# Performance work log

Measured on AMD Instinct MI355X. Metric: run time of the kernel, lower is better.

Reference implementation:

```python
import jax, jax.numpy as jnp
from jax import lax
import numpy as np

N, C, T, V = 32, 64, 300, 25   # batch, channels, frames, joints
INTER = 16                     # out_channels // coff_embedding (64//4)
NS = 3                         # num_subset
K = 9                          # temporal kernel size
EPS = 1e-5                     # torch BatchNorm2d default eps


def _bn(x, g, b):
    # training-mode BatchNorm2d over (N, T, V) per channel, biased variance
    m = x.mean(axis=(0, 2, 3), keepdims=True)
    v = x.var(axis=(0, 2, 3), keepdims=True)
    return (x - m) * lax.rsqrt(v + EPS) * g[None, :, None, None] + b[None, :, None, None]


def setup_inputs() -> dict:
    key = jax.random.key(0)
    ks = jax.random.split(key, 8)
    rn = lambda k, shape, sc=0.05: jax.random.normal(k, shape, jnp.float32) * sc
    x = jax.random.normal(ks[0], (N, C, T, V), jnp.float32)
    A = jax.random.uniform(ks[1], (NS, V, V), dtype=jnp.float32)
    PA = jnp.full((NS, V, V), 1e-6, jnp.float32)   # learned adjacency offset (init 1e-6)
    Wa = rn(ks[2], (NS, INTER, C)); ba = jnp.zeros((NS, INTER), jnp.float32)
    Wb = rn(ks[3], (NS, INTER, C)); bb = jnp.zeros((NS, INTER), jnp.float32)
    Wd = rn(ks[4], (NS, C, C));     bd = jnp.zeros((NS, C), jnp.float32)
    g1 = jnp.ones((C,), jnp.float32); b1 = jnp.zeros((C,), jnp.float32)
    Wt = rn(ks[5], (C, C, K, 1));   bt = jnp.zeros((C,), jnp.float32)
    g2 = jnp.ones((C,), jnp.float32); b2 = jnp.zeros((C,), jnp.float32)
    return dict(x=x, A=A, PA=PA, Wa=Wa, ba=ba, Wb=Wb, bb=bb, Wd=Wd, bd=bd,
                g1=g1, b1=b1, Wt=Wt, bt=bt, g2=g2, b2=b2)


def reference(x, A, PA, Wa, ba, Wb, bb, Wd, bd, g1, b1, Wt, bt, g2, b2):
    n, c, t, v = x.shape
    Au = A + PA                      # effective adjacency per subset, [NS,V,V]
    scale = 1.0 / (INTER * t)        # A1.size(-1)
    x_flat = x.reshape(n, c * t, v)  # [N, C*T, V]
    y = None
    for i in range(NS):
        # 1x1 convs -> embeddings, [N, INTER, T, V]
        a = jnp.einsum('nctv,oc->notv', x, Wa[i]) + ba[i][None, :, None, None]
        b = jnp.einsum('nctv,oc->notv', x, Wb[i]) + bb[i][None, :, None, None]
        A1 = a.transpose(0, 3, 1, 2).reshape(n, v, INTER * t)  # [N, V, INTER*T]
        A2 = b.reshape(n, INTER * t, v)                        # [N, INTER*T, V]
        attn = jax.nn.softmax(jnp.matmul(A1, A2) * scale, axis=-2) + Au[i]  # [N,V,V]
        z = jnp.matmul(x_flat, attn).reshape(n, c, t, v)       # aggregate over joints
        z = jnp.einsum('nctv,oc->notv', z, Wd[i]) + bd[i][None, :, None, None]
        y = z if y is None else y + z
    y = jax.nn.relu(_bn(y, g1, b1) + x)      # gcn bn + identity down + relu
    # temporal conv (9,1), pad (4,0), stride 1, then BN
    yc = lax.conv_general_dilated(y, Wt, window_strides=(1, 1),
                                  padding=((K // 2, K // 2), (0, 0)),
                                  dimension_numbers=('NCHW', 'OIHW', 'NCHW'))
    yc = _bn(yc + bt[None, :, None, None], g2, b2)
    return jax.nn.relu(yc + x)               # identity residual (in==out, stride 1)
```

## Files before the change

### kernel.cpp

```cpp
#include <hip/hip_runtime.h>
#include <hip/hip_bf16.h>

#define NB 32
#define CH 64
#define TF 300
#define VJ 25
#define NSUB 3
#define ICB 16
#define KW 9
#define EPSB 1e-5f

#define TVsz (TF*VJ)
#define CTVsz (CH*TF*VJ)
#define TOTAL (NB*CTVsz)
#define PCCOUNT (NB*TF*VJ)

#define ATC 32
#define ATCN 10

typedef __attribute__((ext_vector_type(8))) short s16x8;
typedef __attribute__((ext_vector_type(4))) float f32x4;

__device__ __forceinline__ unsigned short f2bf(float v) {
    __hip_bfloat16 h = __float2bfloat16(v);
    return *(unsigned short*)&h;
}
__device__ __forceinline__ float bf2f(unsigned int u) {
    return __uint_as_float(u << 16);
}

__global__ void k_prep(const float* __restrict__ Wt, const float* __restrict__ Wd,
                       const float* __restrict__ Wa, const float* __restrict__ ba,
                       const float* __restrict__ Wb, const float* __restrict__ bb,
                       unsigned short* __restrict__ awT, unsigned short* __restrict__ wdcat,
                       unsigned short* __restrict__ wcat, float* __restrict__ biascat) {
    int e = blockIdx.x * 256 + threadIdx.x;
    if (e < CH*CH*KW) {
        int o = e / (CH*KW), c = (e / KW) % CH, k = e % KW;
        awT[(k*CH + o)*CH + c] = f2bf(Wt[e]);
        return;
    }
    int e2 = e - CH*CH*KW;
    if (e2 < NSUB*CH*CH) { wdcat[e2] = f2bf(Wd[e2]); return; }
    int e3 = e2 - NSUB*CH*CH;
    if (e3 < 6144) {
        int i = e3 / 2048, rm = (e3 >> 6) & 31, c = e3 & 63;
        wcat[e3] = f2bf((rm < 16) ? Wa[(i*ICB + rm)*CH + c] : Wb[(i*ICB + rm - 16)*CH + c]);
        return;
    }
    if (e3 < 6240) {
        int j = e3 - 6144;
        int i = j >> 5, r = j & 31;
        biascat[j] = (r < 16) ? ba[i*ICB + r] : bb[i*ICB + r - 16];
    }
}

__global__ __launch_bounds__(256) void k_xt(const float* __restrict__ x,
                                            unsigned short* __restrict__ xbt,
                                            unsigned short* __restrict__ xbc) {
    __shared__ unsigned short ls[64*66];
    int b = blockIdx.x;
    int n = b / 118, tile = b % 118;
    int tv0 = tile * 64;
    int tid = threadIdx.x;
    const float* xg = x + (long)n * CTVsz;
    for (int e = tid; e < 1024; e += 256) {
        int c = e >> 4, t4 = (e & 15) * 4;
        int tv = tv0 + t4;
        if (tv < TVsz) {
            float4 v = *(const float4*)(xg + (long)c*TVsz + tv);
            unsigned short h0 = f2bf(v.x), h1 = f2bf(v.y), h2 = f2bf(v.z), h3 = f2bf(v.w);
            ls[(t4+0)*66 + c] = h0;
            ls[(t4+1)*66 + c] = h1;
            ls[(t4+2)*66 + c] = h2;
            ls[(t4+3)*66 + c] = h3;
            *(uint2*)&xbc[((long)n*CH + c)*TVsz + tv] =
                make_uint2((unsigned)h0 | ((unsigned)h1 << 16),
                           (unsigned)h2 | ((unsigned)h3 << 16));
        }
    }
    __syncthreads();
    for (int e = tid; e < 1024; e += 256) {
        int tvl = e >> 4, c4 = (e & 15) * 4;
        int tv = tv0 + tvl;
        if (tv < TVsz) {
            unsigned int lo = *(const unsigned int*)&ls[tvl*66 + c4];
            unsigned int hi = *(const unsigned int*)&ls[tvl*66 + c4 + 2];
            *(uint2*)&xbt[((long)n*TVsz + tv)*CH + c4] = make_uint2(lo, hi);
        }
    }
}

__global__ __launch_bounds__(256) void k_attn(
    const unsigned short* __restrict__ xbt, const unsigned short* __restrict__ wcat,
    const float* __restrict__ biascat, float* __restrict__ Mbuf)
{
    __shared__ __align__(16) char emb[32*32*ATC*2];
    __shared__ float gram[625];
    int b = blockIdx.x;
    int i   = b / (NB*ATCN);
    int rem = b % (NB*ATCN);
    int n = rem / ATCN, tc = rem % ATCN;
    int t0 = tc * ATC;
    int tid = threadIdx.x;
    int wv = tid >> 6, l = tid & 63, l15 = l & 15, lhi = l >> 4;

    for (int e = tid; e < 625; e += 256) gram[e] = 0.f;

    s16x8 wf[2][2];
    #pragma unroll
    for (int mf = 0; mf < 2; ++mf)
        #pragma unroll
        for (int kc = 0; kc < 2; ++kc)
            wf[mf][kc] = *(const s16x8*)(wcat + ((i*32 + mf*16 + l15)*64 + kc*32 + lhi*8));
    float bs[2][4];
    #pragma unroll
    for (int mf = 0; mf < 2; ++mf)
        #pragma unroll
        for (int r = 0; r < 4; ++r)
            bs[mf][r] = biascat[i*32 + mf*16 + lhi*4 + r];

    const unsigned short* xb = xbt + (long)n * TVsz * CH;
    for (int v = wv; v < 25; v += 4) {
        f32x4 ae[2][2];
        #pragma unroll
        for (int mf = 0; mf < 2; ++mf)
            #pragma unroll
            for (int nf = 0; nf < 2; ++nf)
                ae[mf][nf] = (f32x4){0.f,0.f,0.f,0.f};
        #pragma unroll
        for (int nf = 0; nf < 2; ++nf) {
            int t = t0 + nf*16 + l15;
            int tcl = t < TF ? t : TF-1;
            const unsigned short* bp = xb + ((long)tcl*VJ + v)*CH;
            s16x8 b0 = *(const s16x8*)(bp + lhi*8);
            s16x8 b1 = *(const s16x8*)(bp + 32 + lhi*8);
            #pragma unroll
            for (int mf = 0; mf < 2; ++mf) {
                ae[mf][nf] = __builtin_amdgcn_mfma_f32_16x16x32_bf16(wf[mf][0], b0, ae[mf][nf], 0,0,0);
                ae[mf][nf] = __builtin_amdgcn_mfma_f32_16x16x32_bf16(wf[mf][1], b1, ae[mf][nf], 0,0,0);
            }
        }
        #pragma unroll
        for (int mf = 0; mf < 2; ++mf)
            #pragma unroll
            for (int nf = 0; nf < 2; ++nf)
                #pragma unroll
                for (int r = 0; r < 4; ++r) {
                    int t  = t0 + nf*16 + l15;
                    int tl = nf*16 + l15;
                    int m  = mf*16 + lhi*4 + r;
                    float val = (t < TF) ? (ae[mf][nf][r] + bs[mf][r]) : 0.f;
                    int byte = (((v*32 + m)*ATC + tl)*2) ^ ((v&7)<<4);
                    *(unsigned short*)(emb + byte) = f2bf(val);
                }
    }
    __syncthreads();

    f32x4 ag[2][2];
    #pragma unroll
    for (int mu = 0; mu < 2; ++mu)
        #pragma unroll
        for (int nw = 0; nw < 2; ++nw)
            ag[mu][nw] = (f32x4){0.f,0.f,0.f,0.f};
    #pragma unroll
    for (int oo = 0; oo < 4; ++oo) {
        int o = wv*4 + oo;
        s16x8 fa[2], fb[2];
        #pragma unroll
        for (int mu = 0; mu < 2; ++mu) {
            int u = mu*16 + l15; if (u > 24) u = 24;
            fa[mu] = *(const s16x8*)(emb + ((((u*32 + o)*ATC + lhi*8)*2) ^ ((u&7)<<4)));
        }
        #pragma unroll
        for (int nw = 0; nw < 2; ++nw) {
            int w = nw*16 + l15; if (w > 24) w = 24;
            fb[nw] = *(const s16x8*)(emb + ((((w*32 + 16 + o)*ATC + lhi*8)*2) ^ ((w&7)<<4)));
        }
        #pragma unroll
        for (int mu = 0; mu < 2; ++mu)
            #pragma unroll
            for (int nw = 0; nw < 2; ++nw)
                ag[mu][nw] = __builtin_amdgcn_mfma_f32_16x16x32_bf16(fa[mu], fb[nw], ag[mu][nw], 0,0,0);
    }
    #pragma unroll
    for (int mu = 0; mu < 2; ++mu)
        #pragma unroll
        for (int nw = 0; nw < 2; ++nw)
            #pragma unroll
            for (int r = 0; r < 4; ++r) {
                int u = mu*16 + lhi*4 + r;
                int w = nw*16 + l15;
                if (u < 25 && w < 25)
                    atomicAdd(&gram[u*25 + w], ag[mu][nw][r]);
            }
    __syncthreads();
    for (int e = tid; e < 625; e += 256)
        atomicAdd(&Mbuf[(i*NB + n)*625 + e], gram[e]);
}

__global__ void k_softmax(const float* __restrict__ A, const float* __restrict__ PA,
                          const float* __restrict__ Mbuf,
                          unsigned short* __restrict__ attnbf) {
    int b = blockIdx.x;
    int i = b / NB, n = b % NB;
    int w = threadIdx.x;
    unsigned short* row = attnbf + (((long)n*NSUB + i)*32 + w)*40;
    if (w >= 25) {
        if (w < 32) {
            #pragma unroll
            for (int u = 0; u < 40; ++u) row[u] = 0;
        }
        return;
    }
    const float* M = Mbuf + b*625;
    const float scale = 1.0f / (float)(ICB * TF);
    float col[25];
    float mx = -1e30f;
    #pragma unroll
    for (int u = 0; u < 25; ++u) { col[u] = M[u*25 + w] * scale; mx = fmaxf(mx, col[u]); }
    float s = 0.f;
    #pragma unroll
    for (int u = 0; u < 25; ++u) { col[u] = __expf(col[u] - mx); s += col[u]; }
    float inv = 1.0f / s;
    #pragma unroll
    for (int u = 0; u < 25; ++u)
        row[u] = f2bf(col[u]*inv + A[i*625 + u*25 + w] + PA[i*625 + u*25 + w]);
    #pragma unroll
    for (int u = 25; u < 40; ++u) row[u] = 0;
}

__global__ __launch_bounds__(256) void k_yz(
    const unsigned short* __restrict__ xbc, const unsigned short* __restrict__ attnbf,
    const unsigned short* __restrict__ wdcat, const float* __restrict__ bd,
    unsigned short* __restrict__ ybuf, float* __restrict__ s1, float* __restrict__ s2)
{
    __shared__ __align__(16) unsigned short attnT[NSUB*32*40];
    __shared__ float ss[64], sq[64];

    int b = blockIdx.x;
    int n = b / 75, tq = b % 75;
    int tid = threadIdx.x;
    int wv = tid >> 6, l = tid & 63, l15 = l & 15, lhi = l >> 4;

    if (tid < 64) { ss[tid] = 0.f; sq[tid] = 0.f; }
    {
        const uint4* srcp = (const uint4*)(attnbf + (long)n * (NSUB*32*40));
        uint4* dstp = (uint4*)attnT;
        for (int e = tid; e < 480; e += 256) dstp[e] = srcp[e];
    }
    __syncthreads();

    int tg = tq*4 + wv;
    const unsigned short* xr = xbc + (long)n*CTVsz + tg*25;
    s16x8 afx[4];
    #pragma unroll
    for (int mf = 0; mf < 4; ++mf)
        afx[mf] = *(const s16x8*)(xr + (long)(mf*16 + l15)*TVsz + lhi*8);

    f32x4 acc2[4][2];
    #pragma unroll
    for (int mf = 0; mf < 4; ++mf)
        #pragma unroll
        for (int nf = 0; nf < 2; ++nf)
            acc2[mf][nf] = (f32x4){0.f,0.f,0.f,0.f};

    int srcA4 = (l15 + 32*(lhi & 1)) << 2;
    int srcB4 = srcA4 + 64;
    bool hsel = (lhi & 2) != 0;

    const f32x4 zero4 = (f32x4){0.f,0.f,0.f,0.f};
    for (int i = 0; i < NSUB; ++i) {
        s16x8 bfa0 = *(const s16x8*)(attnT + (i*32 + l15)*40 + lhi*8);
        s16x8 bfa1 = *(const s16x8*)(attnT + (i*32 + 16 + l15)*40 + lhi*8);
        f32x4 zacc[4][2];
        #pragma unroll
        for (int mf = 0; mf < 4; ++mf) {
            zacc[mf][0] = __builtin_amdgcn_mfma_f32_16x16x32_bf16(afx[mf], bfa0, zero4, 0,0,0);
            zacc[mf][1] = __builtin_amdgcn_mfma_f32_16x16x32_bf16(afx[mf], bfa1, zero4, 0,0,0);
        }
        unsigned pk[4][2][2];
        #pragma unroll
        for (int mf = 0; mf < 4; ++mf)
            #pragma unroll
            for (int nf = 0; nf < 2; ++nf) {
                pk[mf][nf][0] = (unsigned)f2bf(zacc[mf][nf][0]) | ((unsigned)f2bf(zacc[mf][nf][1]) << 16);
                pk[mf][nf][1] = (unsigned)f2bf(zacc[mf][nf][2]) | ((unsigned)f2bf(zacc[mf][nf][3]) << 16);
            }
        #pragma unroll
        for (int kc = 0; kc < 2; ++kc) {
            s16x8 bz[2];
            #pragma unroll
            for (int nf = 0; nf < 2; ++nf) {
                unsigned dw0, dw1, dw2, dw3;
                {
                    unsigned a0 = (unsigned)__builtin_amdgcn_ds_bpermute(srcA4, (int)pk[kc*2+0][nf][0]);
                    unsigned a1 = (unsigned)__builtin_amdgcn_ds_bpermute(srcA4, (int)pk[kc*2+1][nf][0]);
                    unsigned b0 = (unsigned)__builtin_amdgcn_ds_bpermute(srcB4, (int)pk[kc*2+0][nf][0]);
                    unsigned b1 = (unsigned)__builtin_amdgcn_ds_bpermute(srcB4, (int)pk[kc*2+1][nf][0]);
                    dw0 = hsel ? a1 : a0;
                    dw2 = hsel ? b1 : b0;
                }
                {
                    unsigned a0 = (unsigned)__builtin_amdgcn_ds_bpermute(srcA4, (int)pk[kc*2+0][nf][1]);
                    unsigned a1 = (unsigned)__builtin_amdgcn_ds_bpermute(srcA4, (int)pk[kc*2+1][nf][1]);
                    unsigned b0 = (unsigned)__builtin_amdgcn_ds_bpermute(srcB4, (int)pk[kc*2+0][nf][1]);
                    unsigned b1 = (unsigned)__builtin_amdgcn_ds_bpermute(srcB4, (int)pk[kc*2+1][nf][1]);
                    dw1 = hsel ? a1 : a0;
                    dw3 = hsel ? b1 : b0;
                }
                union { s16x8 v; unsigned u[4]; } tmp;
                tmp.u[0] = dw0; tmp.u[1] = dw1; tmp.u[2] = dw2; tmp.u[3] = dw3;
                bz[nf] = tmp.v;
            }
            #pragma unroll
            for (int mf2 = 0; mf2 < 4; ++mf2) {
                s16x8 afw = *(const s16x8*)(wdcat + ((i*CH + mf2*16 + l15)*CH + kc*32 + lhi*8));
                acc2[mf2][0] = __builtin_amdgcn_mfma_f32_16x16x32_bf16(afw, bz[0], acc2[mf2][0], 0,0,0);
                acc2[mf2][1] = __builtin_amdgcn_mfma_f32_16x16x32_bf16(afw, bz[1], acc2[mf2][1], 0,0,0);
            }
        }
    }

    #pragma unroll
    for (int mf = 0; mf < 4; ++mf) {
        #pragma unroll
        for (int r = 0; r < 4; ++r) {
            int o = mf*16 + lhi*4 + r;
            float bds = bd[o] + bd[CH + o] + bd[2*CH + o];
            float p = 0.f, q = 0.f;
            #pragma unroll
            for (int nf = 0; nf < 2; ++nf) {
                int v = nf*16 + l15;
                if (v < VJ) {
                    float val = acc2[mf][nf][r] + bds;
                    ybuf[((long)n*CH + o)*TVsz + tg*25 + v] = f2bf(val);
                    p += val; q += val*val;
                }
            }
            p += __shfl_xor(p, 1, 64); q += __shfl_xor(q, 1, 64);
            p += __shfl_xor(p, 2, 64); q += __shfl_xor(q, 2, 64);
            p += __shfl_xor(p, 4, 64); q += __shfl_xor(q, 4, 64);
            p += __shfl_xor(p, 8, 64); q += __shfl_xor(q, 8, 64);
            if (l15 == 0) { atomicAdd(&ss[o], p); atomicAdd(&sq[o], q); }
        }
    }
    __syncthreads();
    if (tid < 64) { atomicAdd(&s1[tid], ss[tid]); atomicAdd(&s2[tid], sq[tid]); }
}

__global__ __launch_bounds__(256) void k_bn1t(
    const float* __restrict__ x, const float* __restrict__ g1, const float* __restrict__ b1,
    const float* __restrict__ s1, const float* __restrict__ s2,
    const unsigned short* __restrict__ yb, unsigned short* __restrict__ ybt)
{
    __shared__ unsigned short ls[64*66];
    int b = blockIdx.x;
    int n = b / 118, tile = b % 118;
    int tv0 = tile * 64;
    const float invN = 1.0f / (float)PCCOUNT;
    int tid = threadIdx.x;

    for (int e = tid; e < 1024; e += 256) {
        int c = e >> 4, t4 = (e & 15) * 4;
        int tv = tv0 + t4;
        if (tv < TVsz) {
            long gbase = (long)n*CTVsz + (long)c*TVsz;
            float m  = s1[c] * invN;
            float vr = s2[c] * invN - m*m;
            float sc = rsqrtf(vr + EPSB) * g1[c];
            float bc = b1[c];
            uint2 yv = *(const uint2*)(yb + gbase + tv);
            float4 xv = *(const float4*)(x + gbase + tv);
            ls[(t4+0)*66 + c] = f2bf(fmaxf((bf2f(yv.x & 0xffffu) - m)*sc + bc + xv.x, 0.f));
            ls[(t4+1)*66 + c] = f2bf(fmaxf((bf2f(yv.x >> 16)     - m)*sc + bc + xv.y, 0.f));
            ls[(t4+2)*66 + c] = f2bf(fmaxf((bf2f(yv.y & 0xffffu) - m)*sc + bc + xv.z, 0.f));
            ls[(t4+3)*66 + c] = f2bf(fmaxf((bf2f(yv.y >> 16)     - m)*sc + bc + xv.w, 0.f));
        }
    }
    __syncthreads();
    for (int e = tid; e < 1024; e += 256) {
        int tvl = e >> 4, c4 = (e & 15) * 4;
        int tv = tv0 + tvl;
        if (tv < TVsz) {
            int v = tv % 25, t = tv / 25;
            unsigned int lo = *(const unsigned int*)&ls[tvl*66 + c4];
            unsigned int hi = *(const unsigned int*)&ls[tvl*66 + c4 + 2];
            *(uint2*)&ybt[(((long)n*VJ + v)*TF + t)*CH + c4] = make_uint2(lo, hi);
        }
    }
}

#define TCROWS 316

__global__ __launch_bounds__(256) void k_tconv(
    const unsigned short* __restrict__ ybt, const unsigned short* __restrict__ awT,
    const float* __restrict__ bt, unsigned short* __restrict__ ycb,
    float* __restrict__ s1, float* __restrict__ s2)
{
    __shared__ __align__(16) char ys[TCROWS*128];
    __shared__ float ss[64], sq[64];
    int b = blockIdx.x;
    int n = b / VJ, v = b % VJ;
    int tid = threadIdx.x;
    int wv = tid >> 6, l = tid & 63, l15 = l & 15, lhi = l >> 4;
    if (tid < 64) { ss[tid] = 0.f; sq[tid] = 0.f; }

    const char* src = (const char*)(ybt + (((long)n*VJ + v)*TF)*CH);
    for (int qq = tid; qq < TCROWS*8; qq += 256) {
        int row = qq >> 3;
        int cb  = (qq & 7) << 4;
        int tg = row - 4;
        uint4 val = make_uint4(0u,0u,0u,0u);
        if (tg >= 0 && tg < TF)
            val = *(const uint4*)(src + (long)tg*128 + cb);
        *(uint4*)(ys + row*128 + (cb ^ ((row & 7) << 4))) = val;
    }
    __syncthreads();

    int wt0 = wv * 75;
    const short* aw = (const short*)awT;

    f32x4 acc[4][5];
    #pragma unroll
    for (int mf = 0; mf < 4; ++mf)
        #pragma unroll
        for (int nf = 0; nf < 5; ++nf)
            acc[mf][nf] = (f32x4){0.f,0.f,0.f,0.f};

    for (int tap = 0; tap < KW; ++tap) {
        #pragma unroll
        for (int kc = 0; kc < 2; ++kc) {
            s16x8 af[4], bfr[5];
            #pragma unroll
            for (int mf = 0; mf < 4; ++mf)
                af[mf] = *(const s16x8*)(aw + ((tap*CH + mf*16 + l15)*CH + kc*32 + lhi*8));
            #pragma unroll
            for (int nf = 0; nf < 5; ++nf) {
                int rloc = wt0 + nf*16 + l15 + tap;
                int cb = (kc*64 + lhi*16) ^ ((rloc & 7) << 4);
                bfr[nf] = *(const s16x8*)(ys + rloc*128 + cb);
            }
            #pragma unroll
            for (int mf = 0; mf < 4; ++mf)
                #pragma unroll
                for (int nf = 0; nf < 5; ++nf)
                    acc[mf][nf] = __builtin_amdgcn_mfma_f32_16x16x32_bf16(
                        af[mf], bfr[nf], acc[mf][nf], 0, 0, 0);
        }
    }

    #pragma unroll
    for (int mf = 0; mf < 4; ++mf) {
        #pragma unroll
        for (int r = 0; r < 4; ++r) {
            int o = mf*16 + lhi*4 + r;
            float bo = bt[o];
            float p = 0.f, q = 0.f;
            #pragma unroll
            for (int nf = 0; nf < 5; ++nf) {
                int tle = nf*16 + l15;
                if (tle < 75) {
                    float val = acc[mf][nf][r] + bo;
                    ycb[(((long)n*CH + o)*VJ + v)*TF + wt0 + tle] = f2bf(val);
                    p += val; q += val*val;
                }
            }
            p += __shfl_xor(p, 1, 64); q += __shfl_xor(q, 1, 64);
            p += __shfl_xor(p, 2, 64); q += __shfl_xor(q, 2, 64);
            p += __shfl_xor(p, 4, 64); q += __shfl_xor(q, 4, 64);
            p += __shfl_xor(p, 8, 64); q += __shfl_xor(q, 8, 64);
            if (l15 == 0) { atomicAdd(&ss[o], p); atomicAdd(&sq[o], q); }
        }
    }
    __syncthreads();
    if (tid < 64) { atomicAdd(&s1[tid], ss[tid]); atomicAdd(&s2[tid], sq[tid]); }
}

__global__ __launch_bounds__(256) void k_out(
    const float* __restrict__ x, const float* __restrict__ g2, const float* __restrict__ b2,
    const float* __restrict__ s1, const float* __restrict__ s2,
    const unsigned short* __restrict__ ycb, float* __restrict__ out)
{
    __shared__ float ls[VJ*305];
    const float invN = 1.0f / (float)PCCOUNT;
    int b = blockIdx.x;
    int n = b >> 6, c = b & 63;
    int tid = threadIdx.x;

    float m  = s1[c] * invN;
    float vr = s2[c] * invN - m*m;
    float rs = rsqrtf(vr + EPSB) * g2[c];
    float bc = b2[c];

    const uint2* yc = (const uint2*)(ycb + ((long)n*CH + c)*TVsz);
    for (int e = tid; e < TVsz/4; e += 256) {
        uint2 d = yc[e];
        int base = e*4;
        int v = base / TF, t = base % TF;
        float* lp = &ls[v*305 + t];
        lp[0] = (bf2f(d.x & 0xffffu) - m)*rs + bc;
        lp[1] = (bf2f(d.x >> 16)     - m)*rs + bc;
        lp[2] = (bf2f(d.y & 0xffffu) - m)*rs + bc;
        lp[3] = (bf2f(d.y >> 16)     - m)*rs + bc;
    }
    __syncthreads();

    long gbase = ((long)n*CH + c)*TVsz;
    for (int e = tid; e < TVsz/4; e += 256) {
        int tv = e*4;
        float4 xv = *(const float4*)(x + gbase + tv);
        float4 ov;
        { int v = (tv+0) % 25, t = (tv+0) / 25; ov.x = fmaxf(ls[v*305 + t] + xv.x, 0.f); }
        { int v = (tv+1) % 25, t = (tv+1) / 25; ov.y = fmaxf(ls[v*305 + t] + xv.y, 0.f); }
        { int v = (tv+2) % 25, t = (tv+2) / 25; ov.z = fmaxf(ls[v*305 + t] + xv.z, 0.f); }
        { int v = (tv+3) % 25, t = (tv+3) / 25; ov.w = fmaxf(ls[v*305 + t] + xv.w, 0.f); }
        *(float4*)(out + gbase + tv) = ov;
    }
}

extern "C" void kernel_launch(void* const* d_in, const int* in_sizes, int n_in,
                              void* d_out, int out_size, void* d_ws, size_t ws_size,
                              hipStream_t stream) {
    const float* x  = (const float*)d_in[0];
    const float* A  = (const float*)d_in[1];
    const float* PA = (const float*)d_in[2];
    const float* Wa = (const float*)d_in[3];
    const float* ba = (const float*)d_in[4];
    const float* Wb = (const float*)d_in[5];
    const float* bb = (const float*)d_in[6];
    const float* Wd = (const float*)d_in[7];
    const float* bd = (const float*)d_in[8];
    const float* g1 = (const float*)d_in[9];
    const float* b1 = (const float*)d_in[10];
    const float* Wt = (const float*)d_in[11];
    const float* bt = (const float*)d_in[12];
    const float* g2 = (const float*)d_in[13];
    const float* b2 = (const float*)d_in[14];

    float* ws    = (float*)d_ws;
    float* Mbuf  = ws;
    float* stats = ws + 60000;
    unsigned short* attnbf = (unsigned short*)(ws + 60256);
    unsigned short* wdcat  = (unsigned short*)(ws + 121696);
    unsigned short* wcat   = (unsigned short*)(ws + 127840);
    float* biascat = ws + 130912;
    unsigned short* awT    = (unsigned short*)(ws + 131008);
    unsigned short* xbt    = (unsigned short*)(ws + 149440);
    unsigned short* xbc    = (unsigned short*)(ws + 7829440);
    unsigned short* ybuf   = (unsigned short*)(ws + 15509440);
    unsigned short* ybt = xbt;
    unsigned short* ycb = xbc;

    hipMemsetAsync(Mbuf, 0, (60000 + 256)*sizeof(float), stream);
    k_prep<<<217, 256, 0, stream>>>(Wt, Wd, Wa, ba, Wb, bb, awT, wdcat, wcat, biascat);
    k_xt<<<NB*118, 256, 0, stream>>>(x, xbt, xbc);
    k_attn<<<NSUB*NB*ATCN, 256, 0, stream>>>(xbt, wcat, biascat, Mbuf);
    k_softmax<<<NSUB*NB, 32, 0, stream>>>(A, PA, Mbuf, attnbf);
    k_yz<<<NB*75, 256, 0, stream>>>(xbc, attnbf, wdcat, bd, ybuf, stats, stats + 64);
    k_bn1t<<<NB*118, 256, 0, stream>>>(x, g1, b1, stats, stats + 64, ybuf, ybt);
    k_tconv<<<NB*VJ, 256, 0, stream>>>(ybt, awT, bt, ycb, stats + 128, stats + 192);
    k_out<<<NB*CH, 256, 0, stream>>>(x, g2, b2, stats + 128, stats + 192, ycb, (float*)d_out);
}
```

Baseline: 270.4 us.

## Store GCN output channel-last via LDS and simplify BN1 transpose kernel

k_yz now stages its bf16 output tile in a swizzled LDS buffer and writes ybuf in (n,t,v,c) channel-last order with 16-byte stores, computing per-channel BN statistics from the staged values. Because ybuf already matches the (t,v) ordering, k_bn1t becomes a grid-stride elementwise kernel that reads the bf16 transposed x copy instead of fp32 x and only remaps (t,v) to (v,t) on store. This removes scattered 2-byte global stores and an LDS transpose, and halves residual read traffic, but rounds the identity residual to bf16 and reassigns workspace aliasing.

```diff
diff --git a/kernel.cpp b/kernel.cpp
--- a/kernel.cpp
+++ b/kernel.cpp
@@ -236,14 +236,18 @@
     unsigned short* __restrict__ ybuf, float* __restrict__ s1, float* __restrict__ s2)
 {
     __shared__ __align__(16) unsigned short attnT[NSUB*32*40];
-    __shared__ float ss[64], sq[64];
+    __shared__ __align__(16) unsigned short yl[4*32*64];
+    __shared__ float ss[64], sq[64], bdsum[64];
 
     int b = blockIdx.x;
     int n = b / 75, tq = b % 75;
     int tid = threadIdx.x;
     int wv = tid >> 6, l = tid & 63, l15 = l & 15, lhi = l >> 4;
 
-    if (tid < 64) { ss[tid] = 0.f; sq[tid] = 0.f; }
+    if (tid < 64) {
+        ss[tid] = 0.f; sq[tid] = 0.f;
+        bdsum[tid] = bd[tid] + bd[CH + tid] + bd[2*CH + tid];
+    }
     {
         const uint4* srcp = (const uint4*)(attnbf + (long)n * (NSUB*32*40));
         uint4* dstp = (uint4*)attnT;
@@ -322,72 +326,85 @@
         }
     }
 
-    #pragma unroll
-    for (int mf = 0; mf < 4; ++mf) {
-        #pragma unroll
-        for (int r = 0; r < 4; ++r) {
-            int o = mf*16 + lhi*4 + r;
-            float bds = bd[o] + bd[CH + o] + bd[2*CH + o];
-            float p = 0.f, q = 0.f;
-            #pragma unroll
-            for (int nf = 0; nf < 2; ++nf) {
-                int v = nf*16 + l15;
-                if (v < VJ) {
-                    float val = acc2[mf][nf][r] + bds;
-                    ybuf[((long)n*CH + o)*TVsz + tg*25 + v] = f2bf(val);
-                    p += val; q += val*val;
-                }
-            }
-            p += __shfl_xor(p, 1, 64); q += __shfl_xor(q, 1, 64);
-            p += __shfl_xor(p, 2, 64); q += __shfl_xor(q, 2, 64);
-            p += __shfl_xor(p, 4, 64); q += __shfl_xor(q, 4, 64);
-            p += __shfl_xor(p, 8, 64); q += __shfl_xor(q, 8, 64);
-            if (l15 == 0) { atomicAdd(&ss[o], p); atomicAdd(&sq[o], q); }
-        }
+    float bdr[4][4];
+    #pragma unroll
+    for (int mf = 0; mf < 4; ++mf)
+        #pragma unroll
+        for (int r = 0; r < 4; ++r)
+            bdr[mf][r] = bdsum[mf*16 + lhi*4 + r];
+    #pragma unroll
+    for (int mf = 0; mf < 4; ++mf)
+        #pragma unroll
+        for (int nf = 0; nf < 2; ++nf)
+            #pragma unroll
+            for (int r = 0; r < 4; ++r) {
+                int o = mf*16 + lhi*4 + r;
+                int row = wv*32 + nf*16 + l15;
+                int byte = row*128 + ((o*2) ^ ((row & 7) << 4));
+                *(unsigned short*)((char*)yl + byte) = f2bf(acc2[mf][nf][r] + bdr[mf][r]);
+            }
+    __syncthreads();
+
+    int og = tid & 7, base = tid >> 3;
+    float p[8], q[8];
+    #pragma unroll
+    for (int k = 0; k < 8; ++k) { p[k] = 0.f; q[k] = 0.f; }
+    uint4* dst = (uint4*)ybuf + ((long)n*TVsz + tq*100) * 8;
+    for (int ntv = base; ntv < 100; ntv += 32) {
+        int t = ntv / 25, v = ntv % 25;
+        int row = t*32 + v;
+        int byte = row*128 + ((og*16) ^ ((row & 7) << 4));
+        uint4 d = *(const uint4*)((char*)yl + byte);
+        dst[ntv*8 + og] = d;
+        const unsigned short* hp = (const unsigned short*)&d;
+        #pragma unroll
+        for (int k = 0; k < 8; ++k) {
+            float v2 = bf2f(hp[k]);
+            p[k] += v2; q[k] += v2*v2;
+        }
+    }
+    #pragma unroll
+    for (int k = 0; k < 8; ++k) {
+        atomicAdd(&ss[og*8 + k], p[k]);
+        atomicAdd(&sq[og*8 + k], q[k]);
     }
     __syncthreads();
     if (tid < 64) { atomicAdd(&s1[tid], ss[tid]); atomicAdd(&s2[tid], sq[tid]); }
 }
 
 __global__ __launch_bounds__(256) void k_bn1t(
-    const float* __restrict__ x, const float* __restrict__ g1, const float* __restrict__ b1,
-    const float* __restrict__ s1, const float* __restrict__ s2,
+    const unsigned short* __restrict__ xbt, const float* __restrict__ g1,
+    const float* __restrict__ b1, const float* __restrict__ s1, const float* __restrict__ s2,
     const unsigned short* __restrict__ yb, unsigned short* __restrict__ ybt)
 {
-    __shared__ unsigned short ls[64*66];
-    int b = blockIdx.x;
-    int n = b / 118, tile = b % 118;
-    int tv0 = tile * 64;
     const float invN = 1.0f / (float)PCCOUNT;
-    int tid = threadIdx.x;
-
-    for (int e = tid; e < 1024; e += 256) {
-        int c = e >> 4, t4 = (e & 15) * 4;
-        int tv = tv0 + t4;
-        if (tv < TVsz) {
-            long gbase = (long)n*CTVsz + (long)c*TVsz;
-            float m  = s1[c] * invN;
-            float vr = s2[c] * invN - m*m;
-            float sc = rsqrtf(vr + EPSB) * g1[c];
-            float bc = b1[c];
-            uint2 yv = *(const uint2*)(yb + gbase + tv);
-            float4 xv = *(const float4*)(x + gbase + tv);
-            ls[(t4+0)*66 + c] = f2bf(fmaxf((bf2f(yv.x & 0xffffu) - m)*sc + bc + xv.x, 0.f));
-            ls[(t4+1)*66 + c] = f2bf(fmaxf((bf2f(yv.x >> 16)     - m)*sc + bc + xv.y, 0.f));
-            ls[(t4+2)*66 + c] = f2bf(fmaxf((bf2f(yv.y & 0xffffu) - m)*sc + bc + xv.z, 0.f));
-            ls[(t4+3)*66 + c] = f2bf(fmaxf((bf2f(yv.y >> 16)     - m)*sc + bc + xv.w, 0.f));
-        }
-    }
-    __syncthreads();
-    for (int e = tid; e < 1024; e += 256) {
-        int tvl = e >> 4, c4 = (e & 15) * 4;
-        int tv = tv0 + tvl;
-        if (tv < TVsz) {
-            int v = tv % 25, t = tv / 25;
-            unsigned int lo = *(const unsigned int*)&ls[tvl*66 + c4];
-            unsigned int hi = *(const unsigned int*)&ls[tvl*66 + c4 + 2];
-            *(uint2*)&ybt[(((long)n*VJ + v)*TF + t)*CH + c4] = make_uint2(lo, hi);
-        }
+    int og = threadIdx.x & 7;
+    float m[8], sc[8], bc[8];
+    #pragma unroll
+    for (int k = 0; k < 8; ++k) {
+        int c = og*8 + k;
+        m[k] = s1[c] * invN;
+        float vr = s2[c] * invN - m[k]*m[k];
+        sc[k] = rsqrtf(vr + EPSB) * g1[c];
+        bc[k] = b1[c];
+    }
+    long gstride = ((long)gridDim.x * blockDim.x) >> 3;
+    for (long ntv = ((long)blockIdx.x*256 + threadIdx.x) >> 3; ntv < (long)NB*TVsz; ntv += gstride) {
+        long n = ntv / TVsz;
+        int tv = (int)(ntv % TVsz);
+        int t = tv / 25, v = tv % 25;
+        uint4 yv = *((const uint4*)yb + ntv*8 + og);
+        uint4 xv = *((const uint4*)xbt + ntv*8 + og);
+        const unsigned short* yh = (const unsigned short*)&yv;
+        const unsigned short* xh = (const unsigned short*)&xv;
+        uint4 outv;
+        unsigned short* oh = (unsigned short*)&outv;
+        #pragma unroll
+        for (int k = 0; k < 8; ++k) {
+            float val = (bf2f(yh[k]) - m[k])*sc[k] + bc[k] + bf2f(xh[k]);
+            oh[k] = f2bf(fmaxf(val, 0.f));
+        }
+        *((uint4*)ybt + ((n*VJ + v)*(long)TF + t)*8 + og) = outv;
     }
 }
 
@@ -549,8 +566,8 @@
     unsigned short* xbt    = (unsigned short*)(ws + 149440);
     unsigned short* xbc    = (unsigned short*)(ws + 7829440);
     unsigned short* ybuf   = (unsigned short*)(ws + 15509440);
-    unsigned short* ybt = xbt;
-    unsigned short* ycb = xbc;
+    unsigned short* ybt = xbc;
+    unsigned short* ycb = ybuf;
 
     hipMemsetAsync(Mbuf, 0, (60000 + 256)*sizeof(float), stream);
     k_prep<<<217, 256, 0, stream>>>(Wt, Wd, Wa, ba, Wb, bb, awT, wdcat, wcat, biascat);
@@ -558,7 +575,7 @@
     k_attn<<<NSUB*NB*ATCN, 256, 0, stream>>>(xbt, wcat, biascat, Mbuf);
     k_softmax<<<NSUB*NB, 32, 0, stream>>>(A, PA, Mbuf, attnbf);
     k_yz<<<NB*75, 256, 0, stream>>>(xbc, attnbf, wdcat, bd, ybuf, stats, stats + 64);
-    k_bn1t<<<NB*118, 256, 0, stream>>>(x, g1, b1, stats, stats + 64, ybuf, ybt);
+    k_bn1t<<<2048, 256, 0, stream>>>(xbt, g1, b1, stats, stats + 64, ybuf, ybt);
     k_tconv<<<NB*VJ, 256, 0, stream>>>(ybt, awT, bt, ycb, stats + 128, stats + 192);
     k_out<<<NB*CH, 256, 0, stream>>>(x, g2, b2, stats + 128, stats + 192, ycb, (float*)d_out);
 }
```

Measured after the change: 273.7 us. No clear change (+1.2%).
